# Kernel optimization log

Measured on AMD Instinct MI355X. Metric: run time of the kernel, lower is better.

Reference implementation:

```python
import jax, jax.numpy as jnp
import numpy as np

N = 20000      # nodes
E = 320000     # edges (before self-loops)
F_IN = 50      # PPI num_features
C1 = 256       # per-head channels, conv1/conv2
H1 = 4         # heads, conv1/conv2
C3 = 121       # PPI num_classes, conv3 per-head channels
H3 = 6         # heads, conv3 (concat=False -> mean)


def gat_conv(x, src, dst, W, a_src, a_dst, b, heads, ch, concat, n):
    """PyG-style GATConv with self-loops already included in (src, dst).
    Messages flow src -> dst; softmax is over incoming edges of each dst node."""
    h = (x @ W).reshape(n, heads, ch)                      # [N, H, C]
    es = jnp.sum(h * a_src, axis=-1)                       # [N, H]
    ed = jnp.sum(h * a_dst, axis=-1)                       # [N, H]
    e = jax.nn.leaky_relu(es[src] + ed[dst], 0.2)          # [E', H]
    m = jax.ops.segment_max(e, dst, num_segments=n)        # stable softmax per dst
    e = jnp.exp(e - m[dst])
    denom = jax.ops.segment_sum(e, dst, num_segments=n)
    alpha = e / jnp.maximum(denom[dst], 1e-16)             # [E', H]
    out = jax.ops.segment_sum(alpha[:, :, None] * h[src], dst, num_segments=n)  # [N, H, C]
    out = out.reshape(n, heads * ch) if concat else out.mean(axis=1)
    return out + b


def setup_inputs() -> dict:
    key = jax.random.key(0)
    ks = jax.random.split(key, 16)

    def p(k, shape, fan_in):
        return (jax.random.normal(k, shape, jnp.float32) / np.float32(np.sqrt(fan_in)))

    x = jax.random.normal(ks[0], (N, F_IN), jnp.float32)
    edge_index = jax.random.randint(ks[1], (2, E), 0, N, dtype=jnp.int64)
    D1 = H1 * C1  # 1024
    return dict(
        x=x, edge_index=edge_index,
        W1=p(ks[2], (F_IN, D1), F_IN), a1s=p(ks[3], (H1, C1), C1), a1d=p(ks[4], (H1, C1), C1), b1=jnp.zeros((D1,), jnp.float32),
        Wl1=p(ks[5], (F_IN, D1), F_IN), bl1=jnp.zeros((D1,), jnp.float32),
        W2=p(ks[6], (D1, D1), D1), a2s=p(ks[7], (H1, C1), C1), a2d=p(ks[8], (H1, C1), C1), b2=jnp.zeros((D1,), jnp.float32),
        Wl2=p(ks[9], (D1, D1), D1), bl2=jnp.zeros((D1,), jnp.float32),
        W3=p(ks[10], (D1, H3 * C3), D1), a3s=p(ks[11], (H3, C3), C3), a3d=p(ks[12], (H3, C3), C3), b3=jnp.zeros((C3,), jnp.float32),
        Wl3=p(ks[13], (D1, C3), D1), bl3=jnp.zeros((C3,), jnp.float32),
    )


def reference(x, edge_index, W1, a1s, a1d, b1, Wl1, bl1, W2, a2s, a2d, b2, Wl2, bl2, W3, a3s, a3d, b3, Wl3, bl3):
    n = x.shape[0]
    loop = jnp.arange(n, dtype=edge_index.dtype)           # PyG GATConv adds self-loops
    src = jnp.concatenate([edge_index[0], loop])
    dst = jnp.concatenate([edge_index[1], loop])
    x1 = jax.nn.elu(gat_conv(x, src, dst, W1, a1s, a1d, b1, H1, C1, True, n) + x @ Wl1 + bl1)
    x2 = jax.nn.elu(gat_conv(x1, src, dst, W2, a2s, a2d, b2, H1, C1, True, n) + x1 @ Wl2 + bl2)
    out = gat_conv(x2, src, dst, W3, a3s, a3d, b3, H3, C3, False, n) + x2 @ Wl3 + bl3
    return out
```

## Files before the change

### kernel.cpp

```cpp
#include <hip/hip_runtime.h>
#include <hip/hip_bf16.h>
#include <math.h>

typedef __bf16 bf16;
typedef __attribute__((ext_vector_type(4))) __bf16 bf16x4;
typedef __attribute__((ext_vector_type(8))) __bf16 bf16x8;
typedef __attribute__((ext_vector_type(4))) float f32x4;

#define N_NODES 20000
#define N_EDGES 320000
#define E2 (N_EDGES + N_NODES)
#define F_IN 50
#define D1 1024
#define NP12 2048
#define NP3 896
#define SG 2048
#define KA 320

#define PO_A1S 0
#define PO_A1D 1024
#define PO_B1  2048
#define PO_BL1 3072
#define PO_A2S 4096
#define PO_A2D 5120
#define PO_B2  6144
#define PO_BL2 7168
#define PO_A3S 8192
#define PO_A3D 8918
#define PO_B3  9644
#define PO_BL3 9765
#define PO_END 9886

#define PB_PADX  5000
#define PB_WF1   1280
#define PB_PAR   39
#define PB_LOG1  5000

__device__ __forceinline__ int clampi(int v, int lo, int hi)
{
    return v < lo ? lo : (v > hi ? hi : v);
}

__device__ __forceinline__ float loadf(const void* p, long idx, int isb)
{
    return isb ? (float)((const bf16*)p)[idx] : ((const float*)p)[idx];
}

__device__ __forceinline__ int loadei(const int* ei, long idx, int i64)
{
    return i64 ? ei[2 * idx] : ei[idx];
}

__global__ void k_detect(const int* __restrict__ ei,
                         const unsigned short* __restrict__ xw,
                         int* __restrict__ flags)
{
    if (blockIdx.x != 0 || threadIdx.x != 0) return;
    int allz = 1;
    for (int i = 0; i < 128; ++i)
        if (ei[2 * i + 1] != 0) { allz = 0; break; }
    int inr = 0;
    for (int i = 0; i < 128; ++i) {
        int e = (xw[2 * i] >> 7) & 0xFF;
        if (e >= 100 && e <= 140) inr++;
    }
    flags[0] = allz;
    flags[1] = (inr >= 64) ? 1 : 0;
}

template <bool BACT>
__global__ __launch_bounds__(256) void k_gemm(const bf16* __restrict__ A,
                                              const bf16* __restrict__ Bt,
                                              bf16* __restrict__ C,
                                              int M, int K, int lda, int ldb, int ldc,
                                              int mtiles, int ntiles,
                                              const bf16* __restrict__ bias)
{
    __shared__ bf16 As[128 * 64];
    __shared__ bf16 Bs[128 * 64];

    int id = blockIdx.x;
    int gfull = mtiles >> 3;
    int base  = gfull * 8 * ntiles;
    int x, y;
    if (id < base) {
        int gsz = 8 * ntiles;
        int g = id / gsz;
        int r = id - g * gsz;
        x = g * 8 + (r & 7);
        y = r >> 3;
    } else {
        int rem = mtiles - (gfull << 3);
        int r = id - base;
        x = (gfull << 3) + r % rem;
        y = r / rem;
    }
    const int m0 = x * 128;
    const int n0 = y * 128;

    const int tid  = threadIdx.x;
    const int wave = tid >> 6;
    const int lane = tid & 63;
    const int wm   = (wave >> 1) * 64;
    const int wn   = (wave & 1) * 64;
    const int frow  = lane & 15;

    const int srow = wave * 32 + (lane >> 3);
    const int scol = (((lane & 7) ^ (lane >> 3)) * 8);

    f32x4 acc[4][4];
#pragma unroll
    for (int i = 0; i < 4; ++i)
#pragma unroll
        for (int j = 0; j < 4; ++j)
#pragma unroll
            for (int r = 0; r < 4; ++r) acc[i][j][r] = 0.f;

    for (int k0 = 0; k0 < K; k0 += 64) {
#pragma unroll
        for (int i = 0; i < 4; ++i) {
            int ra = srow + i * 8;
            int ga = m0 + ra; if (ga > M - 1) ga = M - 1;
            __builtin_amdgcn_global_load_lds(
                (const __attribute__((address_space(1))) void*)(A + (size_t)ga * lda + k0 + scol),
                (__attribute__((address_space(3))) void*)(As + wave * 2048 + i * 512),
                16, 0, 0);
            int gb = n0 + ra;
            __builtin_amdgcn_global_load_lds(
                (const __attribute__((address_space(1))) void*)(Bt + (size_t)gb * ldb + k0 + scol),
                (__attribute__((address_space(3))) void*)(Bs + wave * 2048 + i * 512),
                16, 0, 0);
        }
        __syncthreads();
#pragma unroll
        for (int kk = 0; kk < 2; ++kk) {
            const int coff = (((kk * 4 + (lane >> 4)) ^ (frow & 7)) << 3);
            bf16x8 af[4], bfr[4];
#pragma unroll
            for (int i = 0; i < 4; ++i) {
                af[i]  = *(const bf16x8*)(As + (wm + i * 16 + frow) * 64 + coff);
                bfr[i] = *(const bf16x8*)(Bs + (wn + i * 16 + frow) * 64 + coff);
            }
#pragma unroll
            for (int i = 0; i < 4; ++i)
#pragma unroll
                for (int j = 0; j < 4; ++j)
                    acc[i][j] = __builtin_amdgcn_mfma_f32_16x16x32_bf16(af[i], bfr[j], acc[i][j], 0, 0, 0);
        }
        __syncthreads();
    }

#pragma unroll
    for (int i = 0; i < 4; ++i) {
#pragma unroll
        for (int j = 0; j < 4; ++j) {
            int rbase = m0 + wm + i * 16 + (lane >> 4) * 4;
            int col   = n0 + wn + j * 16 + frow;
            if constexpr (BACT) {
                float bv = (float)bias[col];
#pragma unroll
                for (int r = 0; r < 4; ++r) {
                    int row = rbase + r;
                    if (row < M) {
                        float v = acc[i][j][r] + bv;
                        v = (v > 0.f) ? v : (__expf(v) - 1.f);
                        C[(size_t)row * ldc + col] = (bf16)v;
                    }
                }
            } else {
#pragma unroll
                for (int r = 0; r < 4; ++r) {
                    int row = rbase + r;
                    if (row < M) C[(size_t)row * ldc + col] = (bf16)acc[i][j][r];
                }
            }
        }
    }
}

__global__ __launch_bounds__(256) void k_veca(const void* __restrict__ W1,
                                              const void* __restrict__ a1s,
                                              const void* __restrict__ a1d,
                                              const void* __restrict__ b1,
                                              const void* __restrict__ bl1,
                                              float* __restrict__ ws, float* __restrict__ wd,
                                              bf16* __restrict__ bsum,
                                              const int* __restrict__ flags)
{
    const int isb = flags[1];
    const int k = blockIdx.x;
    const int h = threadIdx.x >> 6;
    const int c0 = threadIdx.x & 63;
    float s = 0.f, d = 0.f;
    if (k < F_IN) {
        for (int c = c0; c < 256; c += 64) {
            float wv = loadf(W1, (long)k * D1 + h * 256 + c, isb);
            s += wv * loadf(a1s, h * 256 + c, isb);
            d += wv * loadf(a1d, h * 256 + c, isb);
        }
    }
#pragma unroll
    for (int off = 32; off; off >>= 1) {
        s += __shfl_xor(s, off);
        d += __shfl_xor(d, off);
    }
    if (c0 == 0) { ws[k * 4 + h] = s; wd[k * 4 + h] = d; }
    if (k < 4) {
        int j = k * 256 + threadIdx.x;
        bsum[j] = (bf16)(loadf(b1, j, isb) + loadf(bl1, j, isb));
    }
}

struct P12 { const void* s[12]; };

__global__ __launch_bounds__(256) void k_prep(const void* __restrict__ x,
                                              const void* __restrict__ W1,
                                              const void* __restrict__ Wl1,
                                              P12 ps,
                                              bf16* __restrict__ A2,
                                              bf16* __restrict__ Bt,
                                              bf16* __restrict__ pool,
                                              const float* __restrict__ ws,
                                              const float* __restrict__ wd,
                                              float* __restrict__ es,
                                              float* __restrict__ ed,
                                              const int* __restrict__ flags)
{
    const int isb = flags[1];
    int b = blockIdx.x;

    if (b < PB_PADX) {
        int idx = b * 256 + threadIdx.x;
        int n = idx >> 6, k = idx & 63;
        A2[(size_t)n * KA + 256 + k] = (k < F_IN) ? (bf16)loadf(x, (long)n * F_IN + k, isb)
                                                  : (bf16)0.f;
        return;
    }
    b -= PB_PADX;

    if (b < PB_WF1) {
        int idx = b * 256 + threadIdx.x;
        int j = idx / KA;
        int kp = idx - j * KA;
        float v = 0.f;
        if (kp < 256) {
            int hp = kp >> 6, k = kp & 63;
            if ((j >> 8) == hp && k < F_IN) v = loadf(W1, (long)k * D1 + j, isb);
        } else {
            int k = kp - 256;
            if (k < F_IN) v = loadf(Wl1, (long)k * D1 + j, isb);
        }
        Bt[idx] = (bf16)v;
        return;
    }
    b -= PB_WF1;

    if (b < PB_PAR) {
        const int off[13] = {PO_A1S, PO_A1D, PO_B1, PO_BL1, PO_A2S, PO_A2D, PO_B2,
                             PO_BL2, PO_A3S, PO_A3D, PO_B3, PO_BL3, PO_END};
        int idx = b * 256 + threadIdx.x;
        if (idx < PO_END) {
            int seg = 0;
            while (idx >= off[seg + 1]) seg++;
            pool[idx] = (bf16)loadf(ps.s[seg], idx - off[seg], isb);
        }
        return;
    }
    b -= PB_PAR;

    const int wave = threadIdx.x >> 6;
    const int lane = threadIdx.x & 63;
    const int n = b * 4 + wave;
    if (n >= N_NODES) return;
    float xv = (lane < F_IN) ? loadf(x, (long)n * F_IN + lane, isb) : 0.f;
    f32x4 wsv = *(const f32x4*)(ws + lane * 4);
    f32x4 wdv = *(const f32x4*)(wd + lane * 4);
    float s[4], d[4];
#pragma unroll
    for (int h = 0; h < 4; ++h) { s[h] = xv * wsv[h]; d[h] = xv * wdv[h]; }
#pragma unroll
    for (int off = 32; off; off >>= 1)
#pragma unroll
        for (int h = 0; h < 4; ++h) {
            s[h] += __shfl_xor(s[h], off);
            d[h] += __shfl_xor(d[h], off);
        }
    if (lane == 0) {
#pragma unroll
        for (int h = 0; h < 4; ++h) { es[n * 4 + h] = s[h]; ed[n * 4 + h] = d[h]; }
    }
}

__global__ __launch_bounds__(256) void k_wcatT(const void* __restrict__ Wa,
                                               const void* __restrict__ Wb,
                                               bf16* __restrict__ Bt,
                                               int split, int da, int db,
                                               const int* __restrict__ flags)
{
    __shared__ bf16 T[64][65];
    const int isb = flags[1];
    const int k0 = blockIdx.x * 64;
    const int n0 = blockIdx.y * 64;
    const int r = threadIdx.x >> 6;
    const int c = threadIdx.x & 63;
    const int n = n0 + c;
#pragma unroll
    for (int kk = 0; kk < 16; ++kk) {
        int k = k0 + r + kk * 4;
        float v = 0.f;
        if (n < split)           v = loadf(Wa, (long)k * da + n, isb);
        else if (n < split + db) v = loadf(Wb, (long)k * db + (n - split), isb);
        T[r + kk * 4][c] = (bf16)v;
    }
    __syncthreads();
#pragma unroll
    for (int kk = 0; kk < 16; ++kk) {
        int nn = r + kk * 4;
        Bt[(size_t)(n0 + nn) * 1024 + k0 + c] = T[c][nn];
    }
}

__global__ void k_count(const int* __restrict__ ei, int* __restrict__ cnt,
                        const int* __restrict__ flags)
{
    int e = blockIdx.x * 256 + threadIdx.x;
    if (e >= E2) return;
    int i64 = flags[0];
    int d = (e < N_EDGES) ? loadei(ei, (long)N_EDGES + e, i64) : (e - N_EDGES);
    d = clampi(d, 0, N_NODES - 1);
    atomicAdd(&cnt[d], 1);
}

__global__ __launch_bounds__(256) void k_scan(const int* __restrict__ cnt,
                                              int* __restrict__ rp,
                                              int* __restrict__ cur)
{
    __shared__ int ssum[256];
    int tid = threadIdx.x;
    const int chunk = (N_NODES + 255) / 256;
    int lo = tid * chunk;
    int hi = lo + chunk; if (hi > N_NODES) hi = N_NODES;
    int s = 0;
    for (int i = lo; i < hi; ++i) s += cnt[i];
    ssum[tid] = s;
    __syncthreads();
    if (tid == 0) {
        int run = 0;
        for (int i = 0; i < 256; ++i) { int t = ssum[i]; ssum[i] = run; run += t; }
        rp[N_NODES] = run;
    }
    __syncthreads();
    int run = ssum[tid];
    for (int i = lo; i < hi; ++i) { rp[i] = run; cur[i] = run; run += cnt[i]; }
}

__global__ void k_fill(const int* __restrict__ ei, int* __restrict__ cur,
                       int* __restrict__ ss, const int* __restrict__ flags)
{
    int e = blockIdx.x * 256 + threadIdx.x;
    if (e >= E2) return;
    int i64 = flags[0];
    int s, d;
    if (e < N_EDGES) {
        s = loadei(ei, e, i64);
        d = loadei(ei, (long)N_EDGES + e, i64);
    } else {
        s = e - N_EDGES; d = s;
    }
    s = clampi(s, 0, N_NODES - 1);
    d = clampi(d, 0, N_NODES - 1);
    int pos = atomicAdd(&cur[d], 1);
    if (pos >= 0 && pos < E2) ss[pos] = s;
}

__global__ __launch_bounds__(256) void k_aggx(bf16* __restrict__ A2,
                                              const float* __restrict__ es,
                                              const float* __restrict__ ed,
                                              const int* __restrict__ rp,
                                              const int* __restrict__ ss)
{
    __shared__ float smx[4], sinv[4], sed[4];
    __shared__ float sal[64 * 4];
    __shared__ int   ssrc[64];

    const int n   = blockIdx.x;
    const int tid = threadIdx.x;
    int r0 = clampi(rp[n], 0, E2);
    int r1 = clampi(rp[n + 1], r0, E2);
    const int deg = r1 - r0;

    const int sw = tid >> 5, ln = tid & 31;
    if (sw < 4) {
        int h = sw;
        float edn = ed[n * 4 + h];
        float mx = -1e30f;
        for (int e = ln; e < deg; e += 32) {
            int s = clampi(ss[r0 + e], 0, N_NODES - 1);
            float w = es[s * 4 + h] + edn;
            w = (w > 0.f) ? w : 0.2f * w;
            mx = fmaxf(mx, w);
        }
#pragma unroll
        for (int off = 16; off; off >>= 1) mx = fmaxf(mx, __shfl_xor(mx, off, 32));
        float sm = 0.f;
        for (int e = ln; e < deg; e += 32) {
            int s = clampi(ss[r0 + e], 0, N_NODES - 1);
            float w = es[s * 4 + h] + edn;
            w = (w > 0.f) ? w : 0.2f * w;
            sm += __expf(w - mx);
        }
#pragma unroll
        for (int off = 16; off; off >>= 1) sm += __shfl_xor(sm, off, 32);
        if (ln == 0) { smx[h] = mx; sinv[h] = 1.f / fmaxf(sm, 1e-16f); sed[h] = edn; }
    }
    __syncthreads();

    const int k  = tid & 63;
    const int hh = tid >> 6;
    float acc = 0.f;

    for (int e0 = 0; e0 < deg; e0 += 64) {
        int ce = min(64, deg - e0);
        int ce4 = (ce + 3) & ~3;
        __syncthreads();
        if (tid < ce4 * 4) {
            int e = tid >> 2, h = tid & 3;
            int valid = (e < ce);
            int s = valid ? clampi(ss[r0 + e0 + e], 0, N_NODES - 1) : 0;
            float w = es[s * 4 + h] + sed[h];
            w = (w > 0.f) ? w : 0.2f * w;
            sal[e * 4 + h] = valid ? __expf(w - smx[h]) * sinv[h] : 0.f;
            if (h == 0) ssrc[e] = s;
        }
        __syncthreads();
        for (int e = 0; e < ce4; e += 4) {
            float xv[4], al[4];
#pragma unroll
            for (int p = 0; p < 4; ++p) {
                int s = ssrc[e + p];
                xv[p] = (float)A2[(size_t)s * KA + 256 + k];
            }
#pragma unroll
            for (int p = 0; p < 4; ++p) al[p] = sal[(e + p) * 4 + hh];
#pragma unroll
            for (int p = 0; p < 4; ++p) acc += al[p] * xv[p];
        }
    }
    A2[(size_t)n * KA + hh * 64 + k] = (bf16)acc;
}

template <int H, int C>
__global__ __launch_bounds__(256) void k_logits(const bf16* __restrict__ G,
                                                const bf16* __restrict__ as_,
                                                const bf16* __restrict__ ad_,
                                                float* __restrict__ es, float* __restrict__ ed)
{
    const int wave = threadIdx.x >> 6;
    const int lane = threadIdx.x & 63;
    const int n = blockIdx.x * 4 + wave;
    if (n >= N_NODES) return;

#pragma unroll
    for (int h = 0; h < H; ++h) {
        float s = 0.f, d = 0.f;
        if constexpr (C == 256) {
            bf16x4 g  = *(const bf16x4*)(G + (size_t)n * SG + h * 256 + lane * 4);
            bf16x4 av = *(const bf16x4*)(as_ + h * 256 + lane * 4);
            bf16x4 dv = *(const bf16x4*)(ad_ + h * 256 + lane * 4);
#pragma unroll
            for (int j = 0; j < 4; ++j) {
                float gv = (float)g[j];
                s += gv * (float)av[j];
                d += gv * (float)dv[j];
            }
        } else {
            for (int c = lane; c < C; c += 64) {
                float hv = (float)G[(size_t)n * SG + h * C + c];
                s += hv * (float)as_[h * C + c];
                d += hv * (float)ad_[h * C + c];
            }
        }
#pragma unroll
        for (int off = 32; off; off >>= 1) {
            s += __shfl_xor(s, off);
            d += __shfl_xor(d, off);
        }
        if (lane == 0) { es[n * H + h] = s; ed[n * H + h] = d; }
    }
}

template <int H, int C, bool MEAN, bool ELU, bool EXTOUT>
__global__ __launch_bounds__(256) void k_agg(const bf16* __restrict__ G,
                                             const bf16* __restrict__ S,
                                             const float* __restrict__ es,
                                             const float* __restrict__ ed,
                                             const int* __restrict__ rp,
                                             const int* __restrict__ ss,
                                             const bf16* __restrict__ bgat,
                                             const bf16* __restrict__ bskip,
                                             void* __restrict__ out, int sout,
                                             const int* __restrict__ flags)
{
    constexpr int D  = H * C;
    constexpr int NV = (D + 3) / 4;
    constexpr int CH = 256;
    __shared__ float smx[H], sinv[H], sed[H];
    __shared__ float sal[CH * H];
    __shared__ int   ssrc[CH];

    const int n   = blockIdx.x;
    const int tid = threadIdx.x;
    int r0 = clampi(rp[n], 0, E2);
    int r1 = clampi(rp[n + 1], r0, E2);
    const int deg = r1 - r0;

    const int sw = tid >> 5, ln = tid & 31;
    for (int h = sw; h < H; h += 8) {
        float edn = ed[n * H + h];
        float mx = -1e30f;
        for (int e = ln; e < deg; e += 32) {
            int s = clampi(ss[r0 + e], 0, N_NODES - 1);
            float w = es[s * H + h] + edn;
            w = (w > 0.f) ? w : 0.2f * w;
            mx = fmaxf(mx, w);
        }
#pragma unroll
        for (int off = 16; off; off >>= 1) mx = fmaxf(mx, __shfl_xor(mx, off, 32));
        float sm = 0.f;
        for (int e = ln; e < deg; e += 32) {
            int s = clampi(ss[r0 + e], 0, N_NODES - 1);
            float w = es[s * H + h] + edn;
            w = (w > 0.f) ? w : 0.2f * w;
            sm += __expf(w - mx);
        }
#pragma unroll
        for (int off = 16; off; off >>= 1) sm += __shfl_xor(sm, off, 32);
        if (ln == 0) { smx[h] = mx; sinv[h] = 1.f / fmaxf(sm, 1e-16f); sed[h] = edn; }
    }
    __syncthreads();

    const int c0 = tid * 4;
    const int hA = (c0 < D) ? (c0 / C) : 0;
    const int hB = (c0 + 3 < D) ? ((c0 + 3) / C) : hA;
    int hj1 = ((c0 + 1 < D) ? ((c0 + 1) / C) : hA) == hA;
    int hj2 = ((c0 + 2 < D) ? ((c0 + 2) / C) : hA) == hA;
    const bool active = (tid < NV);

    float acc[4] = {0.f, 0.f, 0.f, 0.f};

    for (int e0 = 0; e0 < deg; e0 += CH) {
        int ce = min(CH, deg - e0);
        int ce4 = (ce + 3) & ~3;
        __syncthreads();
        for (int t = tid; t < ce4 * H; t += 256) {
            int e = t / H, h = t - e * H;
            int valid = (e < ce);
            int s = valid ? clampi(ss[r0 + e0 + e], 0, N_NODES - 1) : 0;
            float w = es[s * H + h] + sed[h];
            w = (w > 0.f) ? w : 0.2f * w;
            sal[e * H + h] = valid ? __expf(w - smx[h]) * sinv[h] : 0.f;
            if (h == 0) ssrc[e] = s;
        }
        __syncthreads();
        if (active) {
            for (int eb = 0; eb < ce4; eb += 4) {
                int sg[4];
#pragma unroll
                for (int p = 0; p < 4; ++p) sg[p] = ssrc[eb + p];
                bf16x4 g[4];
#pragma unroll
                for (int p = 0; p < 4; ++p)
                    g[p] = *(const bf16x4*)(G + (size_t)sg[p] * SG + c0);
                if constexpr (C % 4 == 0) {
                    float a[4];
#pragma unroll
                    for (int p = 0; p < 4; ++p) a[p] = sal[(eb + p) * H + hA];
#pragma unroll
                    for (int p = 0; p < 4; ++p)
#pragma unroll
                        for (int j = 0; j < 4; ++j)
                            acc[j] += a[p] * (float)g[p][j];
                } else {
#pragma unroll
                    for (int p = 0; p < 4; ++p) {
                        float aL = sal[(eb + p) * H + hA];
                        float aH = sal[(eb + p) * H + hB];
                        acc[0] += aL * (float)g[p][0];
                        acc[1] += (hj1 ? aL : aH) * (float)g[p][1];
                        acc[2] += (hj2 ? aL : aH) * (float)g[p][2];
                        acc[3] += aH * (float)g[p][3];
                    }
                }
            }
        }
    }

    const int outbf = EXTOUT ? flags[1] : 1;

    if constexpr (!MEAN) {
        if (active) {
            bf16x4 bg = *(const bf16x4*)(bgat + c0);
            bf16x4 sk = *(const bf16x4*)(S + (size_t)n * SG + c0);
            bf16x4 bs = *(const bf16x4*)(bskip + c0);
            bf16x4 ov;
#pragma unroll
            for (int j = 0; j < 4; ++j) {
                float v = acc[j] + (float)bg[j] + (float)sk[j] + (float)bs[j];
                if (ELU) v = (v > 0.f) ? v : (__expf(v) - 1.f);
                ov[j] = (bf16)v;
            }
            *(bf16x4*)((bf16*)out + (size_t)n * sout + c0) = ov;
        }
    } else {
        __shared__ float sagg[D];
        if (active) {
#pragma unroll
            for (int j = 0; j < 4; ++j) {
                int c = c0 + j;
                if (c < D) sagg[c] = acc[j];
            }
        }
        __syncthreads();
        for (int c = tid; c < C; c += 256) {
            float v = 0.f;
#pragma unroll
            for (int h = 0; h < H; ++h) v += sagg[h * C + c];
            v *= (1.f / H);
            v += (float)bgat[c] + (float)S[(size_t)n * SG + c] + (float)bskip[c];
            if (outbf) ((bf16*)out)[(size_t)n * sout + c] = (bf16)v;
            else       ((float*)out)[(size_t)n * sout + c] = v;
        }
    }
}

extern "C" void kernel_launch(void* const* d_in, const int* in_sizes, int n_in,
                              void* d_out, int out_size, void* d_ws, size_t ws_size,
                              hipStream_t stream)
{
    const void* x   = d_in[0];
    const int*  ei  = (const int*)d_in[1];
    const void* W1  = d_in[2];
    const void* Wl1 = d_in[6];
    const void* W2  = d_in[8];
    const void* Wl2 = d_in[12];
    const void* W3  = d_in[14];
    const void* Wl3 = d_in[18];

    P12 ps;
    ps.s[0] = d_in[3];  ps.s[1] = d_in[4];  ps.s[2] = d_in[5];  ps.s[3] = d_in[7];
    ps.s[4] = d_in[9];  ps.s[5] = d_in[10]; ps.s[6] = d_in[11]; ps.s[7] = d_in[13];
    ps.s[8] = d_in[15]; ps.s[9] = d_in[16]; ps.s[10] = d_in[17]; ps.s[11] = d_in[19];

    char* w = (char*)d_ws;
    auto alloc = [&](size_t bytes) {
        char* p = w;
        w += (bytes + 255) & ~(size_t)255;
        return p;
    };
    int*   flags = (int*)alloc(64);
    int*   cnt   = (int*)alloc((size_t)N_NODES * 4);
    int*   rp    = (int*)alloc((size_t)(N_NODES + 1) * 4);
    int*   cur   = (int*)alloc((size_t)N_NODES * 4);
    int*   ss    = (int*)alloc((size_t)E2 * 4);
    float* es    = (float*)alloc((size_t)N_NODES * 6 * 4);
    float* ed    = (float*)alloc((size_t)N_NODES * 6 * 4);
    bf16*  pool  = (bf16*)alloc((size_t)PO_END * 2);
    float* ws1   = (float*)alloc((size_t)64 * 4 * 4);
    float* wd1   = (float*)alloc((size_t)64 * 4 * 4);
    bf16*  bsum  = (bf16*)alloc((size_t)D1 * 2);
    bf16*  Bt    = (bf16*)alloc((size_t)NP12 * 1024 * 2);
    bf16*  X     = (bf16*)alloc((size_t)N_NODES * D1 * 2);
    bf16*  WS    = (bf16*)alloc((size_t)N_NODES * SG * 2);
    bf16*  A2    = WS;

    k_detect<<<1, 64, 0, stream>>>(ei, (const unsigned short*)x, flags);

    hipMemsetAsync(cnt, 0, N_NODES * 4, stream);
    k_count<<<(E2 + 255) / 256, 256, 0, stream>>>(ei, cnt, flags);
    k_scan<<<1, 256, 0, stream>>>(cnt, rp, cur);
    k_fill<<<(E2 + 255) / 256, 256, 0, stream>>>(ei, cur, ss, flags);

    const dim3 blk(256);
    const int MT = (N_NODES + 127) / 128;

    k_veca<<<64, 256, 0, stream>>>(W1, ps.s[0], ps.s[1], ps.s[2], ps.s[3],
                                   ws1, wd1, bsum, flags);
    k_prep<<<PB_PADX + PB_WF1 + PB_PAR + PB_LOG1, 256, 0, stream>>>(
        x, W1, Wl1, ps, A2, Bt, pool, ws1, wd1, es, ed, flags);
    k_aggx<<<N_NODES, 256, 0, stream>>>(A2, es, ed, rp, ss);
    k_gemm<true><<<MT * (D1 / 128), blk, 0, stream>>>(A2, Bt, X, N_NODES, KA, KA, KA, D1,
                                                      MT, D1 / 128, bsum);

    k_wcatT<<<dim3(16, NP12 / 64), blk, 0, stream>>>(W2, Wl2, Bt, 1024, 1024, 1024, flags);
    k_gemm<false><<<MT * (NP12 / 128), blk, 0, stream>>>(X, Bt, WS, N_NODES, 1024, 1024, 1024, SG,
                                                         MT, NP12 / 128, nullptr);
    k_logits<4, 256><<<N_NODES / 4, 256, 0, stream>>>(WS, pool + PO_A2S, pool + PO_A2D, es, ed);
    k_agg<4, 256, false, true, false><<<N_NODES, 256, 0, stream>>>(
        WS, WS + D1, es, ed, rp, ss, pool + PO_B2, pool + PO_BL2, X, D1, flags);

    k_wcatT<<<dim3(16, NP3 / 64), blk, 0, stream>>>(W3, Wl3, Bt, 726, 726, 121, flags);
    k_gemm<false><<<MT * (NP3 / 128), blk, 0, stream>>>(X, Bt, WS, N_NODES, 1024, 1024, 1024, SG,
                                                        MT, NP3 / 128, nullptr);
    k_logits<6, 121><<<N_NODES / 4, 256, 0, stream>>>(WS, pool + PO_A3S, pool + PO_A3D, es, ed);
    k_agg<6, 121, true, false, true><<<N_NODES, 256, 0, stream>>>(
        WS, WS + 726, es, ed, rp, ss, pool + PO_B3, pool + PO_BL3, d_out, 121, flags);
}
```

Before: 655.7 us.

## Aggregate layer-2 GAT messages with one wavefront per destination node

Adds a specialized layer-2 aggregation kernel that assigns one 64-lane wavefront per node, four nodes per block. Each lane owns 16 channels and the per-head softmax uses an online max/sum across edge chunks. Each step gathers four source rows with 16-byte vector loads to raise memory-level parallelism. This replaces the generic one-block-per-node aggregation, avoiding block-wide syncs and shared-memory staging. The exchange is more registers per lane and wavefront-local shared-memory use.

```diff
diff --git a/kernel.cpp b/kernel.cpp
--- a/kernel.cpp
+++ b/kernel.cpp
@@ -487,6 +487,133 @@
         }
         if (lane == 0) { es[n * H + h] = s; ed[n * H + h] = d; }
     }
+}
+
+__global__ __launch_bounds__(256) void k_aggw(const bf16* __restrict__ G,
+                                              const bf16* __restrict__ S,
+                                              const float* __restrict__ es,
+                                              const float* __restrict__ ed,
+                                              const int* __restrict__ rp,
+                                              const int* __restrict__ ss,
+                                              const bf16* __restrict__ bgat,
+                                              const bf16* __restrict__ bskip,
+                                              bf16* __restrict__ out, int sout)
+{
+    __shared__ float sal[4][4][65];
+    __shared__ int   ssrc[4][64];
+
+    const int w    = threadIdx.x >> 6;
+    const int lane = threadIdx.x & 63;
+    const int n    = blockIdx.x * 4 + w;
+    if (n >= N_NODES) return;
+
+    int r0 = clampi(rp[n], 0, E2);
+    int r1 = clampi(rp[n + 1], r0, E2);
+    const int deg = r1 - r0;
+
+    f32x4 edn = *(const f32x4*)(ed + n * 4);
+
+    float mx[4] = {-1e30f, -1e30f, -1e30f, -1e30f};
+    float sm[4] = {0.f, 0.f, 0.f, 0.f};
+    for (int c0 = 0; c0 < deg; c0 += 64) {
+        const int e = c0 + lane;
+        const bool val = (e < deg);
+        const int s = val ? clampi(ss[r0 + e], 0, N_NODES - 1) : 0;
+        f32x4 esv = *(const f32x4*)(es + s * 4);
+        float w4[4], mc[4];
+#pragma unroll
+        for (int h = 0; h < 4; ++h) {
+            float v = esv[h] + edn[h];
+            v = (v > 0.f) ? v : 0.2f * v;
+            w4[h] = val ? v : -1e30f;
+            mc[h] = w4[h];
+        }
+#pragma unroll
+        for (int off = 32; off; off >>= 1)
+#pragma unroll
+            for (int h = 0; h < 4; ++h) mc[h] = fmaxf(mc[h], __shfl_xor(mc[h], off));
+        float ps[4];
+#pragma unroll
+        for (int h = 0; h < 4; ++h) {
+            float mn = fmaxf(mx[h], mc[h]);
+            float f  = __expf(mx[h] - mn);
+            ps[h] = __expf(w4[h] - mn);
+            mx[h] = mn;
+            sm[h] *= f;
+        }
+#pragma unroll
+        for (int off = 32; off; off >>= 1)
+#pragma unroll
+            for (int h = 0; h < 4; ++h) ps[h] += __shfl_xor(ps[h], off);
+#pragma unroll
+        for (int h = 0; h < 4; ++h) sm[h] += ps[h];
+    }
+    float sinv[4];
+#pragma unroll
+    for (int h = 0; h < 4; ++h) sinv[h] = 1.f / fmaxf(sm[h], 1e-16f);
+
+    const int myh  = lane >> 4;
+    const int c0ch = lane * 16;
+    float acc[16];
+#pragma unroll
+    for (int j = 0; j < 16; ++j) acc[j] = 0.f;
+
+    for (int c0 = 0; c0 < deg; c0 += 64) {
+        const int ce = min(64, deg - c0);
+        const bool val = (lane < ce);
+        const int e = c0 + lane;
+        const int s = val ? clampi(ss[r0 + e], 0, N_NODES - 1) : 0;
+        f32x4 esv = *(const f32x4*)(es + s * 4);
+#pragma unroll
+        for (int h = 0; h < 4; ++h) {
+            float v = esv[h] + edn[h];
+            v = (v > 0.f) ? v : 0.2f * v;
+            sal[w][h][lane] = val ? __expf(v - mx[h]) * sinv[h] : 0.f;
+        }
+        ssrc[w][lane] = s;
+        const int ce4 = (ce + 3) & ~3;
+        for (int eb = 0; eb < ce4; eb += 4) {
+            int sg[4]; float a[4];
+#pragma unroll
+            for (int p = 0; p < 4; ++p) {
+                sg[p] = ssrc[w][eb + p];
+                a[p]  = sal[w][myh][eb + p];
+            }
+            bf16x8 g0[4], g1[4];
+#pragma unroll
+            for (int p = 0; p < 4; ++p) {
+                const bf16* gp = G + (size_t)sg[p] * SG + c0ch;
+                g0[p] = *(const bf16x8*)gp;
+                g1[p] = *(const bf16x8*)(gp + 8);
+            }
+#pragma unroll
+            for (int p = 0; p < 4; ++p) {
+#pragma unroll
+                for (int j = 0; j < 8; ++j) acc[j]     += a[p] * (float)g0[p][j];
+#pragma unroll
+                for (int j = 0; j < 8; ++j) acc[j + 8] += a[p] * (float)g1[p][j];
+            }
+        }
+    }
+
+    bf16x8 bg0 = *(const bf16x8*)(bgat + c0ch);
+    bf16x8 bg1 = *(const bf16x8*)(bgat + c0ch + 8);
+    bf16x8 sk0 = *(const bf16x8*)(S + (size_t)n * SG + c0ch);
+    bf16x8 sk1 = *(const bf16x8*)(S + (size_t)n * SG + c0ch + 8);
+    bf16x8 bs0 = *(const bf16x8*)(bskip + c0ch);
+    bf16x8 bs1 = *(const bf16x8*)(bskip + c0ch + 8);
+    bf16x8 ov0, ov1;
+#pragma unroll
+    for (int j = 0; j < 8; ++j) {
+        float v = acc[j] + (float)bg0[j] + (float)sk0[j] + (float)bs0[j];
+        v = (v > 0.f) ? v : (__expf(v) - 1.f);
+        ov0[j] = (bf16)v;
+        float u = acc[j + 8] + (float)bg1[j] + (float)sk1[j] + (float)bs1[j];
+        u = (u > 0.f) ? u : (__expf(u) - 1.f);
+        ov1[j] = (bf16)u;
+    }
+    *(bf16x8*)(out + (size_t)n * sout + c0ch)     = ov0;
+    *(bf16x8*)(out + (size_t)n * sout + c0ch + 8) = ov1;
 }
 
 template <int H, int C, bool MEAN, bool ELU, bool EXTOUT>
@@ -695,8 +822,8 @@
     k_gemm<false><<<MT * (NP12 / 128), blk, 0, stream>>>(X, Bt, WS, N_NODES, 1024, 1024, 1024, SG,
                                                          MT, NP12 / 128, nullptr);
     k_logits<4, 256><<<N_NODES / 4, 256, 0, stream>>>(WS, pool + PO_A2S, pool + PO_A2D, es, ed);
-    k_agg<4, 256, false, true, false><<<N_NODES, 256, 0, stream>>>(
-        WS, WS + D1, es, ed, rp, ss, pool + PO_B2, pool + PO_BL2, X, D1, flags);
+    k_aggw<<<N_NODES / 4, 256, 0, stream>>>(
+        WS, WS + D1, es, ed, rp, ss, pool + PO_B2, pool + PO_BL2, X, D1);
 
     k_wcatT<<<dim3(16, NP3 / 64), blk, 0, stream>>>(W3, Wl3, Bt, 726, 726, 121, flags);
     k_gemm<false><<<MT * (NP3 / 128), blk, 0, stream>>>(X, Bt, WS, N_NODES, 1024, 1024, 1024, SG,
```

New measurement: 648.4 us. About the same (-1.1%).
